# Performance work log

Hardware: AMD Instinct MI355X
Metric: run time of the kernel (lower is better)

Reference implementation:

```python
import jax, jax.numpy as jnp
import numpy as np

NUM_GRAPHS = 64
NEG_SLOPE = 0.1


def gcn_conv(x, src, dst, W, b, num_nodes):
    h = x @ W  # [N, out]
    ones = jnp.ones(src.shape[0], dtype=x.dtype)
    deg = jax.ops.segment_sum(ones, dst, num_segments=num_nodes) + 1.0  # +1 self-loop
    dinv = jax.lax.rsqrt(deg)  # deg >= 1 always
    coef = dinv[src] * dinv[dst]  # [E]
    agg = jax.ops.segment_sum(h[src] * coef[:, None], dst, num_segments=num_nodes)
    # self-loop contribution: dinv[i]^2 * h[i]
    out = agg + h * (dinv * dinv)[:, None] + b
    return out


def leaky_relu(x):
    return jnp.where(x >= 0, x, NEG_SLOPE * x)


def global_mean_pool(x, batch, num_graphs):
    s = jax.ops.segment_sum(x, batch, num_segments=num_graphs)
    cnt = jax.ops.segment_sum(jnp.ones(x.shape[0], dtype=x.dtype), batch, num_segments=num_graphs)
    return s / jnp.maximum(cnt, 1.0)[:, None]


def setup_inputs() -> dict:
    key = jax.random.key(0)
    ks = jax.random.split(key, 10)
    N, E, D_IN, D_H, D_OUT, C = 50000, 600000, 128, 128, 128, 16
    x = jax.random.normal(ks[0], (N, D_IN), dtype=jnp.float32)
    edge_index = jax.random.randint(ks[1], (2, E), 0, N, dtype=jnp.int32)
    batch = jnp.sort(jax.random.randint(ks[2], (N,), 0, NUM_GRAPHS, dtype=jnp.int32))
    def glorot(k, shape):
        lim = np.sqrt(6.0 / (shape[0] + shape[1]))
        return jax.random.uniform(k, shape, jnp.float32, -lim, lim)
    W1 = glorot(ks[3], (D_IN, D_H))
    b1 = jnp.zeros((D_H,), jnp.float32)
    W2 = glorot(ks[4], (D_H, D_OUT))
    b2 = jnp.zeros((D_OUT,), jnp.float32)
    Wl = glorot(ks[5], (D_OUT, C))
    bl = jnp.zeros((C,), jnp.float32)
    return {"x": x, "edge_index": edge_index, "batch": batch,
            "W1": W1, "b1": b1, "W2": W2, "b2": b2, "Wl": Wl, "bl": bl}


def reference(x, edge_index, batch, W1, b1, W2, b2, Wl, bl):
    N = x.shape[0]
    src, dst = edge_index[0], edge_index[1]
    h = gcn_conv(x, src, dst, W1, b1, N)
    h = leaky_relu(h)
    h = gcn_conv(h, src, dst, W2, b2, N)
    h = leaky_relu(h)
    g = global_mean_pool(h, batch, NUM_GRAPHS)  # [G, D_OUT]
    # dropout p=0.2 is identity in eval mode
    return g @ Wl + bl
```

## Files before the change

kernel.cpp:

```cpp
#include <hip/hip_runtime.h>

#define D 128
#define NG 64
#define NC 16
#define NEG 0.1f

typedef __attribute__((ext_vector_type(8))) short bf16x8;
typedef __attribute__((ext_vector_type(4))) float f32x4;

__device__ __forceinline__ float bf2f(unsigned int u16) {
    union { unsigned int i; float f; } c;
    c.i = u16 << 16;
    return c.f;
}
__device__ __forceinline__ unsigned short f2bf(float f) {
    union { float f; unsigned int i; } c;
    c.f = f;
    unsigned int i = c.i;
    unsigned int r = (i + 0x7FFFu + ((i >> 16) & 1u)) >> 16;
    return (unsigned short)r;
}

__global__ void deg_kernel(const int* __restrict__ dst, int* __restrict__ deg, int E) {
    int e = blockIdx.x * blockDim.x + threadIdx.x;
    if (e < E) atomicAdd(&deg[dst[e]], 1);
}

__global__ void prep_w_kernel(const float* __restrict__ W, unsigned short* __restrict__ Wh,
                              unsigned short* __restrict__ Wl) {
    int idx = blockIdx.x * 256 + threadIdx.x;
    int k = idx >> 7, n = idx & 127;
    float x = W[idx];
    unsigned short hi = f2bf(x);
    unsigned short lo = f2bf(x - bf2f(hi));
    Wh[n * 128 + k] = hi;
    Wl[n * 128 + k] = lo;
}

__global__ void scan_block_kernel(const int* __restrict__ deg, int* __restrict__ scan1,
                                  int* __restrict__ blocksum, float* __restrict__ dinv, int N) {
    __shared__ int sm[256];
    int tid = threadIdx.x;
    int i = blockIdx.x * 256 + tid;
    int v = (i < N) ? deg[i] : 0;
    if (i < N) dinv[i] = 1.0f / sqrtf((float)v + 1.0f);
    sm[tid] = v;
    __syncthreads();
    for (int off = 1; off < 256; off <<= 1) {
        int t = (tid >= off) ? sm[tid - off] : 0;
        __syncthreads();
        sm[tid] += t;
        __syncthreads();
    }
    if (i < N) scan1[i] = sm[tid];
    if (tid == 255) blocksum[blockIdx.x] = sm[255];
}

__global__ void scan_tops_kernel(const int* __restrict__ blocksum, int* __restrict__ blockoff,
                                 int nb) {
    __shared__ int sm[256];
    int tid = threadIdx.x;
    int v = (tid < nb) ? blocksum[tid] : 0;
    sm[tid] = v;
    __syncthreads();
    for (int off = 1; off < 256; off <<= 1) {
        int t = (tid >= off) ? sm[tid - off] : 0;
        __syncthreads();
        sm[tid] += t;
        __syncthreads();
    }
    blockoff[tid] = sm[tid] - v;
}

__global__ void finalize_ptr_kernel(const int* __restrict__ deg, const int* __restrict__ scan1,
                                    const int* __restrict__ blockoff, int* __restrict__ ptr,
                                    int N, int E) {
    int i = blockIdx.x * blockDim.x + threadIdx.x;
    if (i < N) {
        ptr[i] = scan1[i] - deg[i] + blockoff[i >> 8];
        if (i == N - 1) ptr[N] = E;
    }
}

__global__ void scatter_kernel(const int* __restrict__ src, const int* __restrict__ dst,
                               const int* __restrict__ ptr, int* __restrict__ fill,
                               const float* __restrict__ dinv,
                               int* __restrict__ csr_src, float* __restrict__ csr_coef, int E) {
    int e = blockIdx.x * blockDim.x + threadIdx.x;
    if (e < E) {
        int d = dst[e];
        int s = src[e];
        int pos = ptr[d] + atomicAdd(&fill[d], 1);
        csr_src[pos] = s;
        csr_coef[pos] = dinv[s] * dinv[d];
    }
}

template <bool AF32>
__global__ __launch_bounds__(256) void gemm_mfma_kernel(const void* __restrict__ Ap,
                                                        const unsigned short* __restrict__ Wh,
                                                        const unsigned short* __restrict__ Wl,
                                                        unsigned int* __restrict__ C, int N) {
    __shared__ unsigned short WsH[128 * 136];
    __shared__ unsigned short WsL[128 * 136];
    int tid = threadIdx.x;
    int w = tid >> 6, lane = tid & 63;
    int quad = lane >> 4, m = lane & 15;
    int rowstart = blockIdx.x * 64;

    {
        const uint4* GH = (const uint4*)Wh;
        const uint4* GL = (const uint4*)Wl;
        uint4* LH = (uint4*)WsH;
        uint4* LL = (uint4*)WsL;
#pragma unroll
        for (int i = 0; i < 8; i++) {
            int li = tid + 256 * i;
            int r = li >> 4, c = li & 15;
            LH[r * 17 + c] = GH[li];
            LL[r * 17 + c] = GL[li];
        }
    }

    int arow = rowstart + 16 * w + m;
    bool valid = arow < N;
    bf16x8 af[4];
    if (AF32) {
        const float* Ag = (const float*)Ap;
#pragma unroll
        for (int kc = 0; kc < 4; kc++) {
            float4 f0 = make_float4(0.f, 0.f, 0.f, 0.f), f1 = f0;
            if (valid) {
                const float4* p = (const float4*)(Ag + (size_t)arow * 128 + kc * 32 + quad * 8);
                f0 = p[0];
                f1 = p[1];
            }
            bf16x8 a;
            a[0] = (short)f2bf(f0.x); a[1] = (short)f2bf(f0.y);
            a[2] = (short)f2bf(f0.z); a[3] = (short)f2bf(f0.w);
            a[4] = (short)f2bf(f1.x); a[5] = (short)f2bf(f1.y);
            a[6] = (short)f2bf(f1.z); a[7] = (short)f2bf(f1.w);
            af[kc] = a;
        }
    } else {
        const unsigned short* Ag = (const unsigned short*)Ap;
#pragma unroll
        for (int kc = 0; kc < 4; kc++) {
            bf16x8 a;
#pragma unroll
            for (int j = 0; j < 8; j++) a[j] = 0;
            if (valid) a = *(const bf16x8*)(Ag + (size_t)arow * 128 + kc * 32 + quad * 8);
            af[kc] = a;
        }
    }
    __syncthreads();

    f32x4 acc[8];
#pragma unroll
    for (int t = 0; t < 8; t++) acc[t] = (f32x4){0.f, 0.f, 0.f, 0.f};

#pragma unroll
    for (int t = 0; t < 8; t++) {
#pragma unroll
        for (int kc = 0; kc < 4; kc++) {
            int off = (t * 16 + m) * 136 + kc * 32 + quad * 8;
            bf16x8 bh = *(const bf16x8*)&WsH[off];
            bf16x8 blo = *(const bf16x8*)&WsL[off];
            acc[t] = __builtin_amdgcn_mfma_f32_16x16x32_bf16(af[kc], bh, acc[t], 0, 0, 0);
            acc[t] = __builtin_amdgcn_mfma_f32_16x16x32_bf16(af[kc], blo, acc[t], 0, 0, 0);
        }
    }

#pragma unroll
    for (int t = 0; t < 8; t++) {
#pragma unroll
        for (int r = 0; r < 4; r++) {
            int row = rowstart + 16 * w + quad * 4 + r;
            unsigned int us = f2bf(acc[t][r]);
            unsigned int other = (unsigned int)__shfl_xor((int)us, 1);
            if (((m & 1) == 0) && row < N)
                C[(size_t)row * 64 + t * 8 + (m >> 1)] = us | (other << 16);
        }
    }
}

__global__ void combine_kernel(const uint4* __restrict__ h4, const int* __restrict__ ptr,
                               const int* __restrict__ csr_src, const float* __restrict__ csr_coef,
                               const float* __restrict__ dinv, const float* __restrict__ b,
                               uint4* __restrict__ out4, int N) {
    int wave = threadIdx.x >> 6;
    int lane = threadIdx.x & 63;
    int i = blockIdx.x * 4 + wave;
    if (i >= N) return;
    int q = lane >> 4;
    int l16 = lane & 15;

    int lo = ptr[i], hi = ptr[i + 1];

    float a0 = 0.f, a1 = 0.f, a2 = 0.f, a3 = 0.f, a4 = 0.f, a5 = 0.f, a6 = 0.f, a7 = 0.f;

    int e = lo + q;
    for (; e + 4 < hi; e += 8) {
        int s0 = csr_src[e];
        int s1 = csr_src[e + 4];
        float c0 = csr_coef[e];
        float c1 = csr_coef[e + 4];
        uint4 v0 = h4[(size_t)s0 * 16 + l16];
        uint4 v1 = h4[(size_t)s1 * 16 + l16];
        a0 += bf2f(v0.x & 0xffffu) * c0; a1 += bf2f(v0.x >> 16) * c0;
        a2 += bf2f(v0.y & 0xffffu) * c0; a3 += bf2f(v0.y >> 16) * c0;
        a4 += bf2f(v0.z & 0xffffu) * c0; a5 += bf2f(v0.z >> 16) * c0;
        a6 += bf2f(v0.w & 0xffffu) * c0; a7 += bf2f(v0.w >> 16) * c0;
        a0 += bf2f(v1.x & 0xffffu) * c1; a1 += bf2f(v1.x >> 16) * c1;
        a2 += bf2f(v1.y & 0xffffu) * c1; a3 += bf2f(v1.y >> 16) * c1;
        a4 += bf2f(v1.z & 0xffffu) * c1; a5 += bf2f(v1.z >> 16) * c1;
        a6 += bf2f(v1.w & 0xffffu) * c1; a7 += bf2f(v1.w >> 16) * c1;
    }
    if (e < hi) {
        int s0 = csr_src[e];
        float c0 = csr_coef[e];
        uint4 v0 = h4[(size_t)s0 * 16 + l16];
        a0 += bf2f(v0.x & 0xffffu) * c0; a1 += bf2f(v0.x >> 16) * c0;
        a2 += bf2f(v0.y & 0xffffu) * c0; a3 += bf2f(v0.y >> 16) * c0;
        a4 += bf2f(v0.z & 0xffffu) * c0; a5 += bf2f(v0.z >> 16) * c0;
        a6 += bf2f(v0.w & 0xffffu) * c0; a7 += bf2f(v0.w >> 16) * c0;
    }
    a0 += __shfl_xor(a0, 16); a0 += __shfl_xor(a0, 32);
    a1 += __shfl_xor(a1, 16); a1 += __shfl_xor(a1, 32);
    a2 += __shfl_xor(a2, 16); a2 += __shfl_xor(a2, 32);
    a3 += __shfl_xor(a3, 16); a3 += __shfl_xor(a3, 32);
    a4 += __shfl_xor(a4, 16); a4 += __shfl_xor(a4, 32);
    a5 += __shfl_xor(a5, 16); a5 += __shfl_xor(a5, 32);
    a6 += __shfl_xor(a6, 16); a6 += __shfl_xor(a6, 32);
    a7 += __shfl_xor(a7, 16); a7 += __shfl_xor(a7, 32);

    float di = dinv[i];
    uint4 sv = h4[(size_t)i * 16 + l16];
    float4 bv0 = ((const float4*)b)[l16 * 2];
    float4 bv1 = ((const float4*)b)[l16 * 2 + 1];
    float dd = di * di;
    float v0 = a0 + bf2f(sv.x & 0xffffu) * dd + bv0.x;
    float v1 = a1 + bf2f(sv.x >> 16) * dd + bv0.y;
    float v2 = a2 + bf2f(sv.y & 0xffffu) * dd + bv0.z;
    float v3 = a3 + bf2f(sv.y >> 16) * dd + bv0.w;
    float v4 = a4 + bf2f(sv.z & 0xffffu) * dd + bv1.x;
    float v5 = a5 + bf2f(sv.z >> 16) * dd + bv1.y;
    float v6 = a6 + bf2f(sv.w & 0xffffu) * dd + bv1.z;
    float v7 = a7 + bf2f(sv.w >> 16) * dd + bv1.w;
    v0 = (v0 >= 0.f) ? v0 : NEG * v0;
    v1 = (v1 >= 0.f) ? v1 : NEG * v1;
    v2 = (v2 >= 0.f) ? v2 : NEG * v2;
    v3 = (v3 >= 0.f) ? v3 : NEG * v3;
    v4 = (v4 >= 0.f) ? v4 : NEG * v4;
    v5 = (v5 >= 0.f) ? v5 : NEG * v5;
    v6 = (v6 >= 0.f) ? v6 : NEG * v6;
    v7 = (v7 >= 0.f) ? v7 : NEG * v7;
    if (q == 0) {
        uint4 pv;
        pv.x = (unsigned int)f2bf(v0) | ((unsigned int)f2bf(v1) << 16);
        pv.y = (unsigned int)f2bf(v2) | ((unsigned int)f2bf(v3) << 16);
        pv.z = (unsigned int)f2bf(v4) | ((unsigned int)f2bf(v5) << 16);
        pv.w = (unsigned int)f2bf(v6) | ((unsigned int)f2bf(v7) << 16);
        out4[(size_t)i * 16 + l16] = pv;
    }
}

__global__ void zero_pool_kernel(float* __restrict__ pooled) {
    pooled[blockIdx.x * 256 + threadIdx.x] = 0.f;
}

#define PROWS 128
__global__ void pool_accum_kernel(const unsigned int* __restrict__ a2,
                                  const int* __restrict__ batch,
                                  float* __restrict__ pooled, int N) {
    int wave = threadIdx.x >> 6;
    int lane = threadIdx.x & 63;
    int start = blockIdx.x * PROWS;
    int end = start + PROWS;
    if (end > N) end = N;
    float s0 = 0.f, s1 = 0.f;
    int curg = -1;
    for (int r = start + wave; r < end; r += 4) {
        int g = batch[r];
        if (g != curg) {
            if (curg >= 0) {
                atomicAdd(&pooled[curg * D + 2 * lane], s0);
                atomicAdd(&pooled[curg * D + 2 * lane + 1], s1);
            }
            curg = g;
            s0 = 0.f;
            s1 = 0.f;
        }
        unsigned int v = a2[(size_t)r * 64 + lane];
        s0 += bf2f(v & 0xffffu);
        s1 += bf2f(v >> 16);
    }
    if (curg >= 0) {
        atomicAdd(&pooled[curg * D + 2 * lane], s0);
        atomicAdd(&pooled[curg * D + 2 * lane + 1], s1);
    }
}

__global__ void final_kernel(const float* __restrict__ pooled, const int* __restrict__ batch,
                             const float* __restrict__ Wl, const float* __restrict__ bl,
                             float* __restrict__ out, int N) {
    int t = blockIdx.x * blockDim.x + threadIdx.x;
    if (t >= NG * NC) return;
    int g = t >> 4, c = t & 15;
    int l = 0, h = N;
    while (l < h) { int m = (l + h) >> 1; if (batch[m] < g) l = m + 1; else h = m; }
    int lo = l;
    h = N;
    while (l < h) { int m = (l + h) >> 1; if (batch[m] < g + 1) l = m + 1; else h = m; }
    int cnt = l - lo;
    float inv = 1.0f / (float)(cnt > 0 ? cnt : 1);
    float dot = 0.f;
    for (int k = 0; k < D; k++) dot += pooled[g * D + k] * Wl[k * NC + c];
    out[t] = dot * inv + bl[c];
}

extern "C" void kernel_launch(void* const* d_in, const int* in_sizes, int n_in,
                              void* d_out, int out_size, void* d_ws, size_t ws_size,
                              hipStream_t stream) {
    const float* x = (const float*)d_in[0];
    const int* ei = (const int*)d_in[1];
    const int* batch = (const int*)d_in[2];
    const float* W1 = (const float*)d_in[3];
    const float* b1 = (const float*)d_in[4];
    const float* W2 = (const float*)d_in[5];
    const float* b2 = (const float*)d_in[6];
    const float* Wlin = (const float*)d_in[7];
    const float* bl = (const float*)d_in[8];
    float* out = (float*)d_out;

    int N = in_sizes[0] / D;
    int E = in_sizes[1] / 2;
    const int* src = ei;
    const int* dst = ei + E;

    float* ws = (float*)d_ws;
    size_t o = 0;
    unsigned int* bufA = (unsigned int*)(ws + o); o += (size_t)N * 64;
    unsigned int* bufB = (unsigned int*)(ws + o); o += (size_t)N * 64;
    int* deg = (int*)(ws + o);      o += N;
    int* fill = (int*)(ws + o);     o += N;
    float* dinv = ws + o;           o += N;
    int* scan1 = (int*)(ws + o);    o += N;
    int* blocksum = (int*)(ws + o); o += 256;
    int* blockoff = (int*)(ws + o); o += 256;
    int* csr_ptr = (int*)(ws + o);  o += (N + 4);
    int* csr_src = (int*)(ws + o);  o += E;
    float* csr_coef = ws + o;       o += E;
    float* pooled = ws + o;         o += NG * D;
    unsigned short* Wt1h = (unsigned short*)(ws + o); o += 8192;
    unsigned short* Wt1l = (unsigned short*)(ws + o); o += 8192;
    unsigned short* Wt2h = (unsigned short*)(ws + o); o += 8192;
    unsigned short* Wt2l = (unsigned short*)(ws + o); o += 8192;

    hipMemsetAsync(deg, 0, (size_t)2 * N * sizeof(int), stream);

    int tb = 256;
    int nscan = (N + 255) / 256;
    prep_w_kernel<<<64, 256, 0, stream>>>(W1, Wt1h, Wt1l);
    prep_w_kernel<<<64, 256, 0, stream>>>(W2, Wt2h, Wt2l);
    deg_kernel<<<(E + tb - 1) / tb, tb, 0, stream>>>(dst, deg, E);
    scan_block_kernel<<<nscan, 256, 0, stream>>>(deg, scan1, blocksum, dinv, N);
    scan_tops_kernel<<<1, 256, 0, stream>>>(blocksum, blockoff, nscan);
    finalize_ptr_kernel<<<nscan, 256, 0, stream>>>(deg, scan1, blockoff, csr_ptr, N, E);
    scatter_kernel<<<(E + tb - 1) / tb, tb, 0, stream>>>(src, dst, csr_ptr, fill, dinv,
                                                         csr_src, csr_coef, E);

    int gblocks = (N + 63) / 64;
    int cblocks = (N + 3) / 4;
    gemm_mfma_kernel<true><<<gblocks, 256, 0, stream>>>(x, Wt1h, Wt1l, (unsigned int*)bufA, N);
    combine_kernel<<<cblocks, 256, 0, stream>>>((const uint4*)bufA, csr_ptr, csr_src, csr_coef,
                                                dinv, b1, (uint4*)bufB, N);
    gemm_mfma_kernel<false><<<gblocks, 256, 0, stream>>>(bufB, Wt2h, Wt2l, (unsigned int*)bufA, N);
    combine_kernel<<<cblocks, 256, 0, stream>>>((const uint4*)bufA, csr_ptr, csr_src, csr_coef,
                                                dinv, b2, (uint4*)bufB, N);
    zero_pool_kernel<<<(NG * D) / 256, 256, 0, stream>>>(pooled);
    pool_accum_kernel<<<(N + PROWS - 1) / PROWS, 256, 0, stream>>>(bufB, batch, pooled, N);
    final_kernel<<<(NG * NC + tb - 1) / tb, tb, 0, stream>>>(pooled, batch, Wlin, bl, out, N);
}
```

Before: 268.2 us.

## Pack CSR edges into int2, read GEMM weights from global, merge prep kernels

Interleaves the source index and coefficient into one int2 array, so the combine loop issues one 8-byte load per edge instead of two separate loads. The GEMM kernel drops its LDS staging of the split bf16 weights and reads them straight from global memory through the cache, which removes the staging copy and the barrier. The two weight-prep launches and the pooled zeroing are merged into one kernel to cut launch count. The risk is that uncached or redundant global weight reads in the GEMM inner loop raise latency compared with LDS reads.

```diff
diff --git a/kernel.cpp b/kernel.cpp
--- a/kernel.cpp
+++ b/kernel.cpp
@@ -26,15 +26,26 @@
     if (e < E) atomicAdd(&deg[dst[e]], 1);
 }
 
-__global__ void prep_w_kernel(const float* __restrict__ W, unsigned short* __restrict__ Wh,
-                              unsigned short* __restrict__ Wl) {
-    int idx = blockIdx.x * 256 + threadIdx.x;
-    int k = idx >> 7, n = idx & 127;
-    float x = W[idx];
-    unsigned short hi = f2bf(x);
-    unsigned short lo = f2bf(x - bf2f(hi));
-    Wh[n * 128 + k] = hi;
-    Wl[n * 128 + k] = lo;
+__global__ void prep_misc_kernel(const float* __restrict__ W1, unsigned short* __restrict__ W1h,
+                                 unsigned short* __restrict__ W1l,
+                                 const float* __restrict__ W2, unsigned short* __restrict__ W2h,
+                                 unsigned short* __restrict__ W2l,
+                                 float* __restrict__ pooled) {
+    int b = blockIdx.x;
+    if (b < 128) {
+        const float* W = (b < 64) ? W1 : W2;
+        unsigned short* Wh = (b < 64) ? W1h : W2h;
+        unsigned short* Wl = (b < 64) ? W1l : W2l;
+        int idx = (b & 63) * 256 + threadIdx.x;
+        int k = idx >> 7, n = idx & 127;
+        float x = W[idx];
+        unsigned short hi = f2bf(x);
+        unsigned short lo = f2bf(x - bf2f(hi));
+        Wh[n * 128 + k] = hi;
+        Wl[n * 128 + k] = lo;
+    } else {
+        pooled[(b - 128) * 256 + threadIdx.x] = 0.f;
+    }
 }
 
 __global__ void scan_block_kernel(const int* __restrict__ deg, int* __restrict__ scan1,
@@ -85,14 +96,14 @@
 __global__ void scatter_kernel(const int* __restrict__ src, const int* __restrict__ dst,
                                const int* __restrict__ ptr, int* __restrict__ fill,
                                const float* __restrict__ dinv,
-                               int* __restrict__ csr_src, float* __restrict__ csr_coef, int E) {
+                               int2* __restrict__ csr_edge, int E) {
     int e = blockIdx.x * blockDim.x + threadIdx.x;
     if (e < E) {
         int d = dst[e];
         int s = src[e];
         int pos = ptr[d] + atomicAdd(&fill[d], 1);
-        csr_src[pos] = s;
-        csr_coef[pos] = dinv[s] * dinv[d];
+        float coef = dinv[s] * dinv[d];
+        csr_edge[pos] = make_int2(s, __float_as_int(coef));
     }
 }
 
@@ -101,26 +112,10 @@
                                                         const unsigned short* __restrict__ Wh,
                                                         const unsigned short* __restrict__ Wl,
                                                         unsigned int* __restrict__ C, int N) {
-    __shared__ unsigned short WsH[128 * 136];
-    __shared__ unsigned short WsL[128 * 136];
     int tid = threadIdx.x;
     int w = tid >> 6, lane = tid & 63;
     int quad = lane >> 4, m = lane & 15;
     int rowstart = blockIdx.x * 64;
-
-    {
-        const uint4* GH = (const uint4*)Wh;
-        const uint4* GL = (const uint4*)Wl;
-        uint4* LH = (uint4*)WsH;
-        uint4* LL = (uint4*)WsL;
-#pragma unroll
-        for (int i = 0; i < 8; i++) {
-            int li = tid + 256 * i;
-            int r = li >> 4, c = li & 15;
-            LH[r * 17 + c] = GH[li];
-            LL[r * 17 + c] = GL[li];
-        }
-    }
 
     int arow = rowstart + 16 * w + m;
     bool valid = arow < N;
@@ -153,7 +148,6 @@
             af[kc] = a;
         }
     }
-    __syncthreads();
 
     f32x4 acc[8];
 #pragma unroll
@@ -163,9 +157,9 @@
     for (int t = 0; t < 8; t++) {
 #pragma unroll
         for (int kc = 0; kc < 4; kc++) {
-            int off = (t * 16 + m) * 136 + kc * 32 + quad * 8;
-            bf16x8 bh = *(const bf16x8*)&WsH[off];
-            bf16x8 blo = *(const bf16x8*)&WsL[off];
+            size_t off = (size_t)(t * 16 + m) * 128 + kc * 32 + quad * 8;
+            bf16x8 bh = *(const bf16x8*)&Wh[off];
+            bf16x8 blo = *(const bf16x8*)&Wl[off];
             acc[t] = __builtin_amdgcn_mfma_f32_16x16x32_bf16(af[kc], bh, acc[t], 0, 0, 0);
             acc[t] = __builtin_amdgcn_mfma_f32_16x16x32_bf16(af[kc], blo, acc[t], 0, 0, 0);
         }
@@ -185,7 +179,7 @@
 }
 
 __global__ void combine_kernel(const uint4* __restrict__ h4, const int* __restrict__ ptr,
-                               const int* __restrict__ csr_src, const float* __restrict__ csr_coef,
+                               const int2* __restrict__ csr_edge,
                                const float* __restrict__ dinv, const float* __restrict__ b,
                                uint4* __restrict__ out4, int N) {
     int wave = threadIdx.x >> 6;
@@ -201,12 +195,12 @@
 
     int e = lo + q;
     for (; e + 4 < hi; e += 8) {
-        int s0 = csr_src[e];
-        int s1 = csr_src[e + 4];
-        float c0 = csr_coef[e];
-        float c1 = csr_coef[e + 4];
-        uint4 v0 = h4[(size_t)s0 * 16 + l16];
-        uint4 v1 = h4[(size_t)s1 * 16 + l16];
+        int2 ed0 = csr_edge[e];
+        int2 ed1 = csr_edge[e + 4];
+        float c0 = __int_as_float(ed0.y);
+        float c1 = __int_as_float(ed1.y);
+        uint4 v0 = h4[(size_t)ed0.x * 16 + l16];
+        uint4 v1 = h4[(size_t)ed1.x * 16 + l16];
         a0 += bf2f(v0.x & 0xffffu) * c0; a1 += bf2f(v0.x >> 16) * c0;
         a2 += bf2f(v0.y & 0xffffu) * c0; a3 += bf2f(v0.y >> 16) * c0;
         a4 += bf2f(v0.z & 0xffffu) * c0; a5 += bf2f(v0.z >> 16) * c0;
@@ -217,9 +211,9 @@
         a6 += bf2f(v1.w & 0xffffu) * c1; a7 += bf2f(v1.w >> 16) * c1;
     }
     if (e < hi) {
-        int s0 = csr_src[e];
-        float c0 = csr_coef[e];
-        uint4 v0 = h4[(size_t)s0 * 16 + l16];
+        int2 ed0 = csr_edge[e];
+        float c0 = __int_as_float(ed0.y);
+        uint4 v0 = h4[(size_t)ed0.x * 16 + l16];
         a0 += bf2f(v0.x & 0xffffu) * c0; a1 += bf2f(v0.x >> 16) * c0;
         a2 += bf2f(v0.y & 0xffffu) * c0; a3 += bf2f(v0.y >> 16) * c0;
         a4 += bf2f(v0.z & 0xffffu) * c0; a5 += bf2f(v0.z >> 16) * c0;
@@ -265,10 +259,6 @@
     }
 }
 
-__global__ void zero_pool_kernel(float* __restrict__ pooled) {
-    pooled[blockIdx.x * 256 + threadIdx.x] = 0.f;
-}
-
 #define PROWS 128
 __global__ void pool_accum_kernel(const unsigned int* __restrict__ a2,
                                   const int* __restrict__ batch,
@@ -349,8 +339,7 @@
     int* blocksum = (int*)(ws + o); o += 256;
     int* blockoff = (int*)(ws + o); o += 256;
     int* csr_ptr = (int*)(ws + o);  o += (N + 4);
-    int* csr_src = (int*)(ws + o);  o += E;
-    float* csr_coef = ws + o;       o += E;
+    int2* csr_edge = (int2*)(ws + o); o += (size_t)2 * E;
     float* pooled = ws + o;         o += NG * D;
     unsigned short* Wt1h = (unsigned short*)(ws + o); o += 8192;
     unsigned short* Wt1l = (unsigned short*)(ws + o); o += 8192;
@@ -361,24 +350,22 @@
 
     int tb = 256;
     int nscan = (N + 255) / 256;
-    prep_w_kernel<<<64, 256, 0, stream>>>(W1, Wt1h, Wt1l);
-    prep_w_kernel<<<64, 256, 0, stream>>>(W2, Wt2h, Wt2l);
+    prep_misc_kernel<<<160, 256, 0, stream>>>(W1, Wt1h, Wt1l, W2, Wt2h, Wt2l, pooled);
     deg_kernel<<<(E + tb - 1) / tb, tb, 0, stream>>>(dst, deg, E);
     scan_block_kernel<<<nscan, 256, 0, stream>>>(deg, scan1, blocksum, dinv, N);
     scan_tops_kernel<<<1, 256, 0, stream>>>(blocksum, blockoff, nscan);
     finalize_ptr_kernel<<<nscan, 256, 0, stream>>>(deg, scan1, blockoff, csr_ptr, N, E);
     scatter_kernel<<<(E + tb - 1) / tb, tb, 0, stream>>>(src, dst, csr_ptr, fill, dinv,
-                                                         csr_src, csr_coef, E);
+                                                         csr_edge, E);
 
     int gblocks = (N + 63) / 64;
     int cblocks = (N + 3) / 4;
     gemm_mfma_kernel<true><<<gblocks, 256, 0, stream>>>(x, Wt1h, Wt1l, (unsigned int*)bufA, N);
-    combine_kernel<<<cblocks, 256, 0, stream>>>((const uint4*)bufA, csr_ptr, csr_src, csr_coef,
+    combine_kernel<<<cblocks, 256, 0, stream>>>((const uint4*)bufA, csr_ptr, csr_edge,
                                                 dinv, b1, (uint4*)bufB, N);
     gemm_mfma_kernel<false><<<gblocks, 256, 0, stream>>>(bufB, Wt2h, Wt2l, (unsigned int*)bufA, N);
-    combine_kernel<<<cblocks, 256, 0, stream>>>((const uint4*)bufA, csr_ptr, csr_src, csr_coef,
+    combine_kernel<<<cblocks, 256, 0, stream>>>((const uint4*)bufA, csr_ptr, csr_edge,
                                                 dinv, b2, (uint4*)bufB, N);
-    zero_pool_kernel<<<(NG * D) / 256, 256, 0, stream>>>(pooled);
     pool_accum_kernel<<<(N + PROWS - 1) / PROWS, 256, 0, stream>>>(bufB, batch, pooled, N);
     final_kernel<<<(NG * NC + tb - 1) / tb, tb, 0, stream>>>(pooled, batch, Wlin, bl, out, N);
 }
```

Result: slower. 309.3 us (+15.4%).
